# Performance work log

Measured on AMD Instinct MI355X. Metric: run time of the kernel, lower is better.

Reference implementation:

```python
import jax, jax.numpy as jnp
import numpy as np

N_NODES = 50000
N_EDGES = 1250000
IN_CH, HID_CH, OUT_CH = 128, 64, 10
N_GRAPHS = 500


def gcn_conv(x, W, src, dst, n_nodes):
    # GCNConv (bias=False, normalize=True, add_self_loops=True):
    # out = D^{-1/2} (A + I) D^{-1/2} X W
    h = x @ W  # [N, H]
    loop = jnp.arange(n_nodes, dtype=src.dtype)
    s = jnp.concatenate([src, loop])
    d = jnp.concatenate([dst, loop])
    deg = jax.ops.segment_sum(jnp.ones_like(d, dtype=h.dtype), d, num_segments=n_nodes)
    dinv = jnp.where(deg > 0, jax.lax.rsqrt(deg), 0.0)
    norm = dinv[s] * dinv[d]  # [E+N]
    msgs = h[s] * norm[:, None]  # gather + normalize
    return jax.ops.segment_sum(msgs, d, num_segments=n_nodes)  # scatter-add


def setup_inputs() -> dict:
    key = jax.random.key(0)
    ks = jax.random.split(key, 8)
    x = jax.random.normal(ks[0], (N_NODES, IN_CH), dtype=jnp.float32)
    edge_index = jax.random.randint(ks[1], (2, N_EDGES), 0, N_NODES, dtype=jnp.int64)
    batch = jnp.sort(jax.random.randint(ks[2], (N_NODES,), 0, N_GRAPHS, dtype=jnp.int64))
    def glorot(k, fan_in, fan_out):
        lim = np.sqrt(6.0 / (fan_in + fan_out))
        return jax.random.uniform(k, (fan_in, fan_out), jnp.float32, -lim, lim)
    W1 = glorot(ks[3], IN_CH, HID_CH)
    W2 = glorot(ks[4], HID_CH, HID_CH)
    W3 = glorot(ks[5], HID_CH, HID_CH)
    Wl = glorot(ks[6], HID_CH, OUT_CH)
    bl = jnp.zeros((OUT_CH,), jnp.float32)
    return {"x": x, "edge_index": edge_index, "batch": batch,
            "W1": W1, "W2": W2, "W3": W3, "Wl": Wl, "bl": bl}


def reference(x, edge_index, batch, W1, W2, W3, Wl, bl):
    src, dst = edge_index[0], edge_index[1]
    n = x.shape[0]
    h = jax.nn.relu(gcn_conv(x, W1, src, dst, n))
    h = jax.nn.relu(gcn_conv(h, W2, src, dst, n))
    h = gcn_conv(h, W3, src, dst, n)
    # global_mean_pool over graph ids
    sums = jax.ops.segment_sum(h, batch, num_segments=N_GRAPHS)
    cnts = jax.ops.segment_sum(jnp.ones((n,), h.dtype), batch, num_segments=N_GRAPHS)
    pooled = sums / jnp.maximum(cnts, 1.0)[:, None]
    return pooled @ Wl + bl
```

## Files before the change

kernel.cpp:

```cpp
#include <hip/hip_runtime.h>

#define CH 64
#define CHUNK 4096
#define BSHIFT 8
#define NBUCK 196

__device__ __forceinline__ unsigned short f2bf_rne(float f) {
    unsigned int u = __float_as_uint(f);
    u += 0x7fffu + ((u >> 16) & 1u);
    return (unsigned short)(u >> 16);
}
__device__ __forceinline__ float bf_lo(unsigned int q) {
    return __uint_as_float(q << 16);
}
__device__ __forceinline__ float bf_hi(unsigned int q) {
    return __uint_as_float(q & 0xffff0000u);
}
__device__ __forceinline__ unsigned int pack2bf(float lo, float hi) {
    return (unsigned int)f2bf_rne(lo) | ((unsigned int)f2bf_rne(hi) << 16);
}

template <int K>
__global__ __launch_bounds__(256) void gemm1_hist_kernel(
        const float* __restrict__ X, const float* __restrict__ W,
        unsigned short* __restrict__ G, int N,
        const int* __restrict__ dst, int* __restrict__ bucket_cnt, int E,
        int gemm_blocks) {
    constexpr int KC  = 64;
    constexpr int XLD = KC + 4;
    __shared__ float Xs[64 * XLD];
    __shared__ float Wls[KC * CH];
    __shared__ int hist[256];
    int tid = threadIdx.x;

    if (blockIdx.x >= gemm_blocks) {
        int cid = blockIdx.x - gemm_blocks;
        int e0 = cid * CHUNK;
        int total = min(CHUNK, E - e0);
        hist[tid] = 0;
        __syncthreads();
        for (int i = tid; i < total; i += 256)
            atomicAdd(&hist[dst[e0 + i] >> BSHIFT], 1);
        __syncthreads();
        if (tid < NBUCK && hist[tid]) atomicAdd(&bucket_cnt[tid], hist[tid]);
        return;
    }

    int tx  = tid & 15;
    int ty  = tid >> 4;
    int row_tile = blockIdx.x * 64;
    int r0 = ty * 4;
    float acc[4][4] = {{0.f}};

    for (int kc = 0; kc < K; kc += KC) {
        __syncthreads();
#pragma unroll
        for (int t = 0; t < 4; ++t) {
            int idx = tid + t * 256;
            int row = idx >> 4;
            int k4  = idx & 15;
            int grow = row_tile + row;
            const float4* xs = (const float4*)(X + (size_t)min(grow, N - 1) * K + kc);
            *(float4*)&Xs[row * XLD + 4 * k4] = xs[k4];
        }
#pragma unroll
        for (int t = 0; t < 4; ++t) {
            int idx = tid + t * 256;
            *(float4*)&Wls[idx * 4] = ((const float4*)(W + (size_t)kc * CH))[idx];
        }
        __syncthreads();
#pragma unroll
        for (int kk = 0; kk < KC; kk += 4) {
            float xr[4][4], wr[4][4];
#pragma unroll
            for (int i = 0; i < 4; ++i) {
                float4 v = *(const float4*)&Xs[(r0 + i) * XLD + kk];
                xr[i][0] = v.x; xr[i][1] = v.y; xr[i][2] = v.z; xr[i][3] = v.w;
            }
#pragma unroll
            for (int j = 0; j < 4; ++j) {
                float4 v = *(const float4*)&Wls[(kk + j) * CH + 4 * tx];
                wr[j][0] = v.x; wr[j][1] = v.y; wr[j][2] = v.z; wr[j][3] = v.w;
            }
#pragma unroll
            for (int i = 0; i < 4; ++i)
#pragma unroll
                for (int j = 0; j < 4; ++j)
#pragma unroll
                    for (int c = 0; c < 4; ++c)
                        acc[i][c] = fmaf(xr[i][j], wr[j][c], acc[i][c]);
        }
    }
#pragma unroll
    for (int i = 0; i < 4; ++i) {
        int r = row_tile + r0 + i;
        if (r < N) {
            ushort4 o;
            o.x = f2bf_rne(acc[i][0]);
            o.y = f2bf_rne(acc[i][1]);
            o.z = f2bf_rne(acc[i][2]);
            o.w = f2bf_rne(acc[i][3]);
            ((ushort4*)G)[(size_t)r * 16 + tx] = o;
        }
    }
}

__global__ __launch_bounds__(256) void scan_gptr_kernel(
        const int* __restrict__ cnt,
        int* __restrict__ bucket_base, int* __restrict__ cursor,
        int* __restrict__ rowptr,
        const int* __restrict__ batch, int* __restrict__ gptr,
        int N, int E, int NG) {
    if (blockIdx.x == 0) {
        __shared__ int sc[256];
        int t = threadIdx.x;
        int c = (t < NBUCK) ? cnt[t] : 0;
        sc[t] = c;
        __syncthreads();
        for (int off = 1; off < 256; off <<= 1) {
            int v = (t >= off) ? sc[t - off] : 0;
            __syncthreads();
            sc[t] += v;
            __syncthreads();
        }
        if (t < NBUCK) { bucket_base[t] = sc[t] - c; cursor[t] = sc[t] - c; }
        if (t == NBUCK - 1) bucket_base[NBUCK] = sc[t];
        if (t == 0) rowptr[N] = E;
    } else {
        for (int g = threadIdx.x; g <= NG; g += 256) {
            if (g == NG) { gptr[NG] = N; continue; }
            int lo = 0, hi = N;
            while (lo < hi) {
                int mid = (lo + hi) >> 1;
                if (batch[mid] < g) lo = mid + 1; else hi = mid;
            }
            gptr[g] = lo;
        }
    }
}

__global__ __launch_bounds__(256) void bin_kernel(
        const int* __restrict__ src, const int* __restrict__ dst,
        int* __restrict__ cursor, unsigned int* __restrict__ pairs, int E) {
    __shared__ unsigned int stage[CHUNK];
    __shared__ int hist[256], sc[256], lbase[256], lcur[256], gbase[256];
    int tid = threadIdx.x;
    int e0 = blockIdx.x * CHUNK;
    int total = min(CHUNK, E - e0);
    hist[tid] = 0;
    __syncthreads();
    for (int i = tid; i < total; i += 256)
        atomicAdd(&hist[dst[e0 + i] >> BSHIFT], 1);
    __syncthreads();
    sc[tid] = hist[tid];
    __syncthreads();
    for (int off = 1; off < 256; off <<= 1) {
        int v = (tid >= off) ? sc[tid - off] : 0;
        __syncthreads();
        sc[tid] += v;
        __syncthreads();
    }
    lbase[tid] = sc[tid] - hist[tid];
    lcur[tid]  = sc[tid] - hist[tid];
    if (tid < NBUCK && hist[tid] > 0) gbase[tid] = atomicAdd(&cursor[tid], hist[tid]);
    __syncthreads();
    for (int i = tid; i < total; i += 256) {
        unsigned int s = (unsigned int)src[e0 + i];
        unsigned int d = (unsigned int)dst[e0 + i];
        int pos = atomicAdd(&lcur[d >> BSHIFT], 1);
        stage[pos] = (d << 16) | s;
    }
    __syncthreads();
    for (int i = tid; i < total; i += 256) {
        unsigned int p = stage[i];
        int b = (int)(p >> 24);
        pairs[gbase[b] + (i - lbase[b])] = p;
    }
}

__global__ __launch_bounds__(256) void bucket_sort_kernel(
        const unsigned int* __restrict__ pairs, const int* __restrict__ base,
        unsigned short* __restrict__ csr, int* __restrict__ rowptr,
        float* __restrict__ dinv, int N) {
    __shared__ int cntl[256], sc[256], cur[256];
    int tid = threadIdx.x;
    int b = blockIdx.x;
    int pbase = base[b], pend = base[b + 1];
    int cnt = pend - pbase;
    cntl[tid] = 0;
    __syncthreads();
    for (int i = tid; i < cnt; i += 256)
        atomicAdd(&cntl[(pairs[pbase + i] >> 16) & 255u], 1);
    __syncthreads();
    sc[tid] = cntl[tid];
    __syncthreads();
    for (int off = 1; off < 256; off <<= 1) {
        int v = (tid >= off) ? sc[tid - off] : 0;
        __syncthreads();
        sc[tid] += v;
        __syncthreads();
    }
    int excl = sc[tid] - cntl[tid];
    cur[tid] = excl;
    int v = (b << BSHIFT) + tid;
    if (v < N) {
        rowptr[v] = pbase + excl;
        dinv[v] = rsqrtf((float)(cntl[tid] + 1));
    }
    __syncthreads();
    for (int i = tid; i < cnt; i += 256) {
        unsigned int p = pairs[pbase + i];
        int pos = atomicAdd(&cur[(p >> 16) & 255u], 1);
        csr[pbase + pos] = (unsigned short)(p & 0xffffu);
    }
}

template <bool PRESCALED, bool F32OUT>
__global__ __launch_bounds__(256) void aggregate_kernel(
        const unsigned short* __restrict__ G, const int* __restrict__ rowptr,
        const unsigned short* __restrict__ csr, const float* __restrict__ dinv,
        void* __restrict__ Out, int N, int E, int relu) {
    int lane = threadIdx.x & 63;
    int w = (blockIdx.x * 256 + threadIdx.x) >> 6;
    int grp = lane >> 3, cl = lane & 7;
    int v = w * 8 + grp;
    bool valid = v < N;
    int vc = valid ? v : N - 1;
    int beg = rowptr[vc];
    int cnt = valid ? rowptr[vc + 1] - beg : 0;
    int mx = cnt;
    mx = max(mx, __shfl_xor(mx, 8));
    mx = max(mx, __shfl_xor(mx, 16));
    mx = max(mx, __shfl_xor(mx, 32));

    const uint4* __restrict__ G4 = (const uint4*)G;
    float a0 = 0.f, a1 = 0.f, a2 = 0.f, a3 = 0.f;
    float a4 = 0.f, a5 = 0.f, a6 = 0.f, a7 = 0.f;
#pragma unroll 2
    for (int it = 0; it < mx; ++it) {
        int eg = min(beg + it, E - 1);
        bool ok = it < cnt;
        int u = ok ? (int)csr[eg] : 0;
        float s;
        if (PRESCALED) s = ok ? 1.f : 0.f;
        else           s = ok ? dinv[u] : 0.f;
        uint4 q = G4[(size_t)u * 8 + cl];
        a0 = fmaf(bf_lo(q.x), s, a0); a1 = fmaf(bf_hi(q.x), s, a1);
        a2 = fmaf(bf_lo(q.y), s, a2); a3 = fmaf(bf_hi(q.y), s, a3);
        a4 = fmaf(bf_lo(q.z), s, a4); a5 = fmaf(bf_hi(q.z), s, a5);
        a6 = fmaf(bf_lo(q.w), s, a6); a7 = fmaf(bf_hi(q.w), s, a7);
    }
    if (valid) {
        uint4 q = G4[(size_t)v * 8 + cl];
        float d = dinv[v];
        float sv = PRESCALED ? 1.f : d;
        float o0 = (a0 + bf_lo(q.x) * sv) * d, o1 = (a1 + bf_hi(q.x) * sv) * d;
        float o2 = (a2 + bf_lo(q.y) * sv) * d, o3 = (a3 + bf_hi(q.y) * sv) * d;
        float o4 = (a4 + bf_lo(q.z) * sv) * d, o5 = (a5 + bf_hi(q.z) * sv) * d;
        float o6 = (a6 + bf_lo(q.w) * sv) * d, o7 = (a7 + bf_hi(q.w) * sv) * d;
        if (relu) {
            o0 = fmaxf(o0, 0.f); o1 = fmaxf(o1, 0.f); o2 = fmaxf(o2, 0.f);
            o3 = fmaxf(o3, 0.f); o4 = fmaxf(o4, 0.f); o5 = fmaxf(o5, 0.f);
            o6 = fmaxf(o6, 0.f); o7 = fmaxf(o7, 0.f);
        }
        if (F32OUT) {
            float4 w0 = {o0, o1, o2, o3}, w1 = {o4, o5, o6, o7};
            ((float4*)Out)[(size_t)v * 16 + cl * 2]     = w0;
            ((float4*)Out)[(size_t)v * 16 + cl * 2 + 1] = w1;
        } else {
            uint4 p;
            p.x = pack2bf(o0, o1); p.y = pack2bf(o2, o3);
            p.z = pack2bf(o4, o5); p.w = pack2bf(o6, o7);
            ((uint4*)Out)[(size_t)v * 8 + cl] = p;
        }
    }
}

__global__ __launch_bounds__(256) void gemm_bf16_kernel(
        const unsigned short* __restrict__ Xbf, const float* __restrict__ W,
        const float* __restrict__ dinv, unsigned short* __restrict__ G, int N) {
    constexpr int XLDU = 36;
    __shared__ unsigned int Xs[64 * XLDU];
    __shared__ float Wls[64 * CH];
    int tid = threadIdx.x;
    int tx  = tid & 15;
    int ty  = tid >> 4;
    int row_tile = blockIdx.x * 64;
    int r0 = ty * 4;
    float acc[4][4] = {{0.f}};

#pragma unroll
    for (int t = 0; t < 2; ++t) {
        int idx = tid + t * 256;
        int row = idx >> 3;
        int k4  = idx & 7;
        int grow = row_tile + row;
        uint4 v = ((const uint4*)Xbf)[(size_t)min(grow, N - 1) * 8 + k4];
        *(uint4*)&Xs[row * XLDU + 4 * k4] = v;
    }
#pragma unroll
    for (int t = 0; t < 4; ++t) {
        int idx = tid + t * 256;
        *(float4*)&Wls[idx * 4] = ((const float4*)W)[idx];
    }
    __syncthreads();
#pragma unroll
    for (int kk = 0; kk < 64; kk += 4) {
        float xr[4][4], wr[4][4];
#pragma unroll
        for (int i = 0; i < 4; ++i) {
            uint2 q = *(const uint2*)&Xs[(r0 + i) * XLDU + (kk >> 1)];
            xr[i][0] = bf_lo(q.x); xr[i][1] = bf_hi(q.x);
            xr[i][2] = bf_lo(q.y); xr[i][3] = bf_hi(q.y);
        }
#pragma unroll
        for (int j = 0; j < 4; ++j) {
            float4 v = *(const float4*)&Wls[(kk + j) * CH + 4 * tx];
            wr[j][0] = v.x; wr[j][1] = v.y; wr[j][2] = v.z; wr[j][3] = v.w;
        }
#pragma unroll
        for (int i = 0; i < 4; ++i)
#pragma unroll
            for (int j = 0; j < 4; ++j)
#pragma unroll
                for (int c = 0; c < 4; ++c)
                    acc[i][c] = fmaf(xr[i][j], wr[j][c], acc[i][c]);
    }
#pragma unroll
    for (int i = 0; i < 4; ++i) {
        int r = row_tile + r0 + i;
        if (r < N) {
            float d = dinv[r];
            ushort4 o;
            o.x = f2bf_rne(acc[i][0] * d);
            o.y = f2bf_rne(acc[i][1] * d);
            o.z = f2bf_rne(acc[i][2] * d);
            o.w = f2bf_rne(acc[i][3] * d);
            ((ushort4*)G)[(size_t)r * 16 + tx] = o;
        }
    }
}

__global__ __launch_bounds__(64) void pool_head_kernel(
        const float* __restrict__ H, const int* __restrict__ gptr,
        const float* __restrict__ Wl, const float* __restrict__ bl,
        float* __restrict__ out, int NG) {
    int g = blockIdx.x;
    int lane = threadIdx.x;
    int s = gptr[g], e = gptr[g + 1];
    float acc = 0.f;
    for (int v = s; v < e; ++v) acc += H[(size_t)v * CH + lane];
    float c = (float)(e - s);
    float mean = (c > 0.f) ? acc / c : 0.f;
    for (int o = 0; o < 10; ++o) {
        float t = mean * Wl[lane * 10 + o];
        for (int off = 32; off > 0; off >>= 1) t += __shfl_down(t, off);
        if (lane == 0) out[g * 10 + o] = t + bl[o];
    }
}

extern "C" void kernel_launch(void* const* d_in, const int* in_sizes, int n_in,
                              void* d_out, int out_size, void* d_ws, size_t ws_size,
                              hipStream_t stream) {
    const float* x     = (const float*)d_in[0];
    const int*   ei    = (const int*)d_in[1];
    const int*   batch = (const int*)d_in[2];
    const float* W1    = (const float*)d_in[3];
    const float* W2    = (const float*)d_in[4];
    const float* W3    = (const float*)d_in[5];
    const float* Wl    = (const float*)d_in[6];
    const float* bl    = (const float*)d_in[7];
    float* out = (float*)d_out;

    const int N  = in_sizes[0] / 128;
    const int E  = in_sizes[1] / 2;
    const int NG = out_size / 10;

    const int* src = ei;
    const int* dst = ei + E;

    const int cb = (E + CHUNK - 1) / CHUNK;

    char* ws = (char*)d_ws;
    size_t off = 0;
    auto alloc = [&](size_t bytes) -> void* {
        void* p = ws + off;
        off += bytes;
        off = (off + 255) & ~(size_t)255;
        return p;
    };
    int*   bucket_cnt  = (int*)alloc((size_t)NBUCK * 4);
    int*   bucket_base = (int*)alloc((size_t)(NBUCK + 1) * 4);
    int*   cursor      = (int*)alloc((size_t)NBUCK * 4);
    unsigned short* csr = (unsigned short*)alloc((size_t)(E + 64) * 2);
    int*   rowptr = (int*)alloc((size_t)(N + 1) * 4);
    float* dinv   = (float*)alloc((size_t)N * 4);
    int*   gptrb  = (int*)alloc((size_t)(NG + 1) * 4);
    unsigned short* GA = (unsigned short*)alloc((size_t)N * CH * 2);
    unsigned short* GB = (unsigned short*)alloc((size_t)N * CH * 2);
    float* hbuf   = (float*)alloc((size_t)N * CH * 4);
    unsigned int* pairs = (unsigned int*)hbuf;

    hipMemsetAsync(bucket_cnt, 0, (size_t)NBUCK * 4, stream);

    int gb = (N + 63) / 64;
    int ab = ((N + 7) / 8 + 3) / 4;

    gemm1_hist_kernel<128><<<gb + cb, 256, 0, stream>>>(x, W1, GA, N,
                                                        dst, bucket_cnt, E, gb);
    scan_gptr_kernel<<<2, 256, 0, stream>>>(bucket_cnt, bucket_base, cursor,
                                            rowptr, batch, gptrb, N, E, NG);
    bin_kernel<<<cb, 256, 0, stream>>>(src, dst, cursor, pairs, E);
    bucket_sort_kernel<<<NBUCK, 256, 0, stream>>>(pairs, bucket_base, csr, rowptr, dinv, N);

    aggregate_kernel<false, false><<<ab, 256, 0, stream>>>(GA, rowptr, csr, dinv,
                                                           GB, N, E, 1);
    gemm_bf16_kernel<<<gb, 256, 0, stream>>>(GB, W2, dinv, GA, N);
    aggregate_kernel<true, false><<<ab, 256, 0, stream>>>(GA, rowptr, csr, dinv,
                                                          GB, N, E, 1);
    gemm_bf16_kernel<<<gb, 256, 0, stream>>>(GB, W3, dinv, GA, N);
    aggregate_kernel<true, true><<<ab, 256, 0, stream>>>(GA, rowptr, csr, dinv,
                                                         hbuf, N, E, 0);

    pool_head_kernel<<<NG, 64, 0, stream>>>(hbuf, gptrb, Wl, bl, out, NG);
}
```

Baseline: 247.5 us.

## Sort nodes by degree for balanced aggregation and split accumulators

After: 514.3 us. +107.8%, slower.

```diff
diff --git a/kernel.cpp b/kernel.cpp
--- a/kernel.cpp
+++ b/kernel.cpp
@@ -181,7 +181,8 @@
 __global__ __launch_bounds__(256) void bucket_sort_kernel(
         const unsigned int* __restrict__ pairs, const int* __restrict__ base,
         unsigned short* __restrict__ csr, int* __restrict__ rowptr,
-        float* __restrict__ dinv, int N) {
+        float* __restrict__ dinv, unsigned char* __restrict__ deg,
+        int* __restrict__ deghist, int N) {
     __shared__ int cntl[256], sc[256], cur[256];
     int tid = threadIdx.x;
     int b = blockIdx.x;
@@ -206,6 +207,9 @@
     if (v < N) {
         rowptr[v] = pbase + excl;
         dinv[v] = rsqrtf((float)(cntl[tid] + 1));
+        int d = min(cntl[tid], 255);
+        deg[v] = (unsigned char)d;
+        atomicAdd(&deghist[d], 1);
     }
     __syncthreads();
     for (int i = tid; i < cnt; i += 256) {
@@ -215,19 +219,46 @@
     }
 }
 
+__global__ __launch_bounds__(256) void deg_scan_kernel(
+        const int* __restrict__ deghist, int* __restrict__ degcur) {
+    __shared__ int sc[256];
+    int t = threadIdx.x;
+    int c = deghist[t];
+    sc[t] = c;
+    __syncthreads();
+    for (int off = 1; off < 256; off <<= 1) {
+        int v = (t >= off) ? sc[t - off] : 0;
+        __syncthreads();
+        sc[t] += v;
+        __syncthreads();
+    }
+    degcur[t] = sc[t] - c;
+}
+
+__global__ __launch_bounds__(256) void perm_kernel(
+        const unsigned char* __restrict__ deg, int* __restrict__ degcur,
+        int* __restrict__ perm, int N) {
+    int v = blockIdx.x * 256 + threadIdx.x;
+    if (v < N) {
+        int p = atomicAdd(&degcur[deg[v]], 1);
+        perm[p] = v;
+    }
+}
+
 template <bool PRESCALED, bool F32OUT>
 __global__ __launch_bounds__(256) void aggregate_kernel(
         const unsigned short* __restrict__ G, const int* __restrict__ rowptr,
         const unsigned short* __restrict__ csr, const float* __restrict__ dinv,
+        const int* __restrict__ perm,
         void* __restrict__ Out, int N, int E, int relu) {
     int lane = threadIdx.x & 63;
     int w = (blockIdx.x * 256 + threadIdx.x) >> 6;
     int grp = lane >> 3, cl = lane & 7;
-    int v = w * 8 + grp;
-    bool valid = v < N;
-    int vc = valid ? v : N - 1;
-    int beg = rowptr[vc];
-    int cnt = valid ? rowptr[vc + 1] - beg : 0;
+    int idx = w * 8 + grp;
+    bool valid = idx < N;
+    int v = perm[valid ? idx : N - 1];
+    int beg = rowptr[v];
+    int cnt = valid ? rowptr[v + 1] - beg : 0;
     int mx = cnt;
     mx = max(mx, __shfl_xor(mx, 8));
     mx = max(mx, __shfl_xor(mx, 16));
@@ -236,20 +267,32 @@
     const uint4* __restrict__ G4 = (const uint4*)G;
     float a0 = 0.f, a1 = 0.f, a2 = 0.f, a3 = 0.f;
     float a4 = 0.f, a5 = 0.f, a6 = 0.f, a7 = 0.f;
-#pragma unroll 2
-    for (int it = 0; it < mx; ++it) {
-        int eg = min(beg + it, E - 1);
-        bool ok = it < cnt;
-        int u = ok ? (int)csr[eg] : 0;
-        float s;
-        if (PRESCALED) s = ok ? 1.f : 0.f;
-        else           s = ok ? dinv[u] : 0.f;
-        uint4 q = G4[(size_t)u * 8 + cl];
-        a0 = fmaf(bf_lo(q.x), s, a0); a1 = fmaf(bf_hi(q.x), s, a1);
-        a2 = fmaf(bf_lo(q.y), s, a2); a3 = fmaf(bf_hi(q.y), s, a3);
-        a4 = fmaf(bf_lo(q.z), s, a4); a5 = fmaf(bf_hi(q.z), s, a5);
-        a6 = fmaf(bf_lo(q.w), s, a6); a7 = fmaf(bf_hi(q.w), s, a7);
-    }
+    float b0 = 0.f, b1 = 0.f, b2 = 0.f, b3 = 0.f;
+    float b4 = 0.f, b5 = 0.f, b6 = 0.f, b7 = 0.f;
+    int nit = (mx + 1) >> 1;
+    for (int it = 0; it < nit; ++it) {
+        int i0 = 2 * it, i1 = i0 + 1;
+        int e0 = min(beg + i0, E - 1);
+        int e1 = min(beg + i1, E - 1);
+        bool ok0 = i0 < cnt, ok1 = i1 < cnt;
+        int u0 = ok0 ? (int)csr[e0] : 0;
+        int u1 = ok1 ? (int)csr[e1] : 0;
+        float s0, s1;
+        if (PRESCALED) { s0 = ok0 ? 1.f : 0.f;        s1 = ok1 ? 1.f : 0.f; }
+        else           { s0 = ok0 ? dinv[u0] : 0.f;   s1 = ok1 ? dinv[u1] : 0.f; }
+        uint4 q0 = G4[(size_t)u0 * 8 + cl];
+        uint4 q1 = G4[(size_t)u1 * 8 + cl];
+        a0 = fmaf(bf_lo(q0.x), s0, a0); a1 = fmaf(bf_hi(q0.x), s0, a1);
+        a2 = fmaf(bf_lo(q0.y), s0, a2); a3 = fmaf(bf_hi(q0.y), s0, a3);
+        a4 = fmaf(bf_lo(q0.z), s0, a4); a5 = fmaf(bf_hi(q0.z), s0, a5);
+        a6 = fmaf(bf_lo(q0.w), s0, a6); a7 = fmaf(bf_hi(q0.w), s0, a7);
+        b0 = fmaf(bf_lo(q1.x), s1, b0); b1 = fmaf(bf_hi(q1.x), s1, b1);
+        b2 = fmaf(bf_lo(q1.y), s1, b2); b3 = fmaf(bf_hi(q1.y), s1, b3);
+        b4 = fmaf(bf_lo(q1.z), s1, b4); b5 = fmaf(bf_hi(q1.z), s1, b5);
+        b6 = fmaf(bf_lo(q1.w), s1, b6); b7 = fmaf(bf_hi(q1.w), s1, b7);
+    }
+    a0 += b0; a1 += b1; a2 += b2; a3 += b3;
+    a4 += b4; a5 += b5; a6 += b6; a7 += b7;
     if (valid) {
         uint4 q = G4[(size_t)v * 8 + cl];
         float d = dinv[v];
@@ -390,37 +433,45 @@
         return p;
     };
     int*   bucket_cnt  = (int*)alloc((size_t)NBUCK * 4);
+    int*   deghist     = (int*)alloc(256 * 4);
     int*   bucket_base = (int*)alloc((size_t)(NBUCK + 1) * 4);
     int*   cursor      = (int*)alloc((size_t)NBUCK * 4);
+    int*   degcur      = (int*)alloc(256 * 4);
     unsigned short* csr = (unsigned short*)alloc((size_t)(E + 64) * 2);
     int*   rowptr = (int*)alloc((size_t)(N + 1) * 4);
     float* dinv   = (float*)alloc((size_t)N * 4);
+    unsigned char* deg = (unsigned char*)alloc((size_t)N);
+    int*   perm   = (int*)alloc((size_t)N * 4);
     int*   gptrb  = (int*)alloc((size_t)(NG + 1) * 4);
     unsigned short* GA = (unsigned short*)alloc((size_t)N * CH * 2);
     unsigned short* GB = (unsigned short*)alloc((size_t)N * CH * 2);
     float* hbuf   = (float*)alloc((size_t)N * CH * 4);
     unsigned int* pairs = (unsigned int*)hbuf;
 
-    hipMemsetAsync(bucket_cnt, 0, (size_t)NBUCK * 4, stream);
+    hipMemsetAsync(bucket_cnt, 0, 2048, stream);
 
     int gb = (N + 63) / 64;
     int ab = ((N + 7) / 8 + 3) / 4;
+    int nb = (N + 255) / 256;
 
     gemm1_hist_kernel<128><<<gb + cb, 256, 0, stream>>>(x, W1, GA, N,
                                                         dst, bucket_cnt, E, gb);
     scan_gptr_kernel<<<2, 256, 0, stream>>>(bucket_cnt, bucket_base, cursor,
                                             rowptr, batch, gptrb, N, E, NG);
     bin_kernel<<<cb, 256, 0, stream>>>(src, dst, cursor, pairs, E);
-    bucket_sort_kernel<<<NBUCK, 256, 0, stream>>>(pairs, bucket_base, csr, rowptr, dinv, N);
+    bucket_sort_kernel<<<NBUCK, 256, 0, stream>>>(pairs, bucket_base, csr, rowptr,
+                                                  dinv, deg, deghist, N);
+    deg_scan_kernel<<<1, 256, 0, stream>>>(deghist, degcur);
+    perm_kernel<<<nb, 256, 0, stream>>>(deg, degcur, perm, N);
 
     aggregate_kernel<false, false><<<ab, 256, 0, stream>>>(GA, rowptr, csr, dinv,
-                                                           GB, N, E, 1);
+                                                           perm, GB, N, E, 1);
     gemm_bf16_kernel<<<gb, 256, 0, stream>>>(GB, W2, dinv, GA, N);
     aggregate_kernel<true, false><<<ab, 256, 0, stream>>>(GA, rowptr, csr, dinv,
-                                                          GB, N, E, 1);
+                                                          perm, GB, N, E, 1);
     gemm_bf16_kernel<<<gb, 256, 0, stream>>>(GB, W3, dinv, GA, N);
     aggregate_kernel<true, true><<<ab, 256, 0, stream>>>(GA, rowptr, csr, dinv,
-                                                         hbuf, N, E, 0);
+                                                         perm, hbuf, N, E, 0);
 
     pool_head_kernel<<<NG, 64, 0, stream>>>(hbuf, gptrb, Wl, bl, out, NG);
 }
```
